# Performance work log

Measured on AMD Instinct MI355X. Metric: run time of the kernel, lower is better.

## Reference

```python
import jax, jax.numpy as jnp
import numpy as np

MIN_V, MAX_V = 1e-7, 10.0
POWER = 2.0
N_NODES = 200000


def _hyper_layer(H, edges, W, b):
    """One HyperTensorGraphConvolution layer (full-neighborhood branch).

    H: [N, d] node signals; edges: [E, S] node indices per hyperedge.
    For each (edge, node_i): power-mean over the other S-1 nodes of the edge,
    divided by (S-1), accumulated onto node_i; then row-normalize and linear.
    """
    N, d = H.shape
    E, S = edges.shape
    H = jnp.clip(H, MIN_V, MAX_V)
    P = H ** POWER                                   # [N, d]
    g = P[edges]                                     # [E, S, d] gather
    edge_sum = g.sum(axis=1, keepdims=True)          # [E, 1, d]
    neigh_mean = (edge_sum - g) / (S - 1)            # exclude self, /(len(nodes)-1)
    contrib = neigh_mean ** (1.0 / POWER)            # [E, S, d]
    add = jax.ops.segment_sum(contrib.reshape(E * S, d),
                              edges.reshape(-1), num_segments=N)
    new_signal = H + add
    # row-normalize (rowsum > 0 because H >= 1e-7)
    rowsum = new_signal.sum(axis=1)
    r_inv = jnp.where(jnp.isfinite(1.0 / rowsum), 1.0 / rowsum, 0.0)
    AH = new_signal * r_inv[:, None]
    return AH @ W + b


def setup_inputs() -> dict:
    key = jax.random.key(0)
    k1, k2, k3, k4, k5, k6 = jax.random.split(key, 6)
    d, h, c = 128, 16, 40
    H = jax.random.uniform(k1, (N_NODES, d), dtype=jnp.float32)
    edges = jax.random.randint(k2, (40000, 16), 0, N_NODES, dtype=jnp.int64)
    std1 = 1.0 / np.sqrt(h)
    std2 = 1.0 / np.sqrt(c)
    W1 = jax.random.uniform(k3, (d, h), jnp.float32, -std1, std1)
    b1 = jax.random.uniform(k4, (h,), jnp.float32, -std1, std1)
    W2 = jax.random.uniform(k5, (h, c), jnp.float32, -std2, std2)
    b2 = jax.random.uniform(k6, (c,), jnp.float32, -std2, std2)
    return {"H": H, "W1": W1, "b1": b1, "W2": W2, "b2": b2, "edges": edges}


def reference(H, W1, b1, W2, b2, edges):
    # layer 1 + relu (dropout is identity in eval mode)
    x = jax.nn.relu(_hyper_layer(H, edges, W1, b1))
    # layer 2
    return _hyper_layer(x, edges, W2, b2)
```

## Files before the change

### kernel.cpp

```cpp
#include <hip/hip_runtime.h>

#define MIN_V 1e-7f
#define MAX_V 10.0f
#define INV15 (1.0f/15.0f)
#define CAP 32

typedef _Float16 half2v __attribute__((ext_vector_type(2)));
typedef _Float16 half4v __attribute__((ext_vector_type(4)));
typedef _Float16 half8v __attribute__((ext_vector_type(8)));

static __device__ __forceinline__ float clipv(float v){
    return fminf(fmaxf(v, MIN_V), MAX_V);
}

__global__ __launch_bounds__(256) void ch_stream(const float* __restrict__ H,
                                                 _Float16* __restrict__ CH, int total8){
    int stride = gridDim.x*256;
    for (int i = blockIdx.x*256 + threadIdx.x; i < total8; i += stride){
        const float4* p = (const float4*)(H + (size_t)i*8);
        float4 a = p[0], b = p[1];
        half8v o;
        o[0]=(_Float16)clipv(a.x); o[1]=(_Float16)clipv(a.y);
        o[2]=(_Float16)clipv(a.z); o[3]=(_Float16)clipv(a.w);
        o[4]=(_Float16)clipv(b.x); o[5]=(_Float16)clipv(b.y);
        o[6]=(_Float16)clipv(b.z); o[7]=(_Float16)clipv(b.w);
        *(half8v*)(CH + (size_t)i*8) = o;
    }
}

__global__ void build_lists(const int* __restrict__ edges, int* __restrict__ cnt,
                            unsigned short* __restrict__ lists, int total){
    int i = blockIdx.x*256 + threadIdx.x;
    if (i >= total) return;
    int node = edges[i];
    int p = atomicAdd(&cnt[node], 1);
    if (p < CAP) lists[(size_t)node*CAP + p] = (unsigned short)(i >> 4);
}

__global__ __launch_bounds__(256) void es_l1(const _Float16* __restrict__ CH,
                                             const int* __restrict__ edges,
                                             _Float16* __restrict__ ES1s, int E){
    int tid = threadIdx.x;
    int hw = tid >> 5, l32 = tid & 31;
    int e = blockIdx.x*8 + hw;
    if (e >= E) return;
    int nid = edges[(size_t)e*16 + (l32 & 15)];
    int dq = l32 * 4;
    float s0=0.f, s1=0.f, s2=0.f, s3=0.f;
    #pragma unroll
    for (int s=0;s<16;++s){
        int idx = __shfl(nid, s, 32);
        half4v v = *(const half4v*)(CH + (size_t)idx*128 + dq);
        float f0=(float)v[0], f1=(float)v[1], f2=(float)v[2], f3=(float)v[3];
        s0 += f0*f0; s1 += f1*f1; s2 += f2*f2; s3 += f3*f3;
    }
    half4v o;
    o[0]=(_Float16)(s0*INV15); o[1]=(_Float16)(s1*INV15);
    o[2]=(_Float16)(s2*INV15); o[3]=(_Float16)(s3*INV15);
    *(half4v*)(ES1s + (size_t)e*128 + dq) = o;
}

__global__ __launch_bounds__(256) void fused_l1(
    const _Float16* __restrict__ CH, const _Float16* __restrict__ ES1s,
    const int* __restrict__ cnt, const unsigned short* __restrict__ lists,
    const float* __restrict__ W1, const float* __restrict__ b1,
    _Float16* __restrict__ X, int N, int EZERO){
    __shared__ _Float16 snw[2][8*128];
    int tid = threadIdx.x;
    int wave = tid >> 6, lane = tid & 63;

    int q = lane >> 4, h = lane & 15;
    half2v w2[16];
    #pragma unroll
    for (int i=0;i<16;++i){
        w2[i][0] = (_Float16)W1[(q*32+2*i  )*16 + h];
        w2[i][1] = (_Float16)W1[(q*32+2*i+1)*16 + h];
    }
    const half2v ones = {(_Float16)1.f, (_Float16)1.f};
    float bv = b1[h];

    int hw = tid >> 5;
    int k32 = tid & 31;
    int dq = k32 * 4;

    const _Float16 i15 = (_Float16)INV15;
    const half4v i15v = {i15, i15, i15, i15};
    const half4v z4 = {(_Float16)0.f,(_Float16)0.f,(_Float16)0.f,(_Float16)0.f};

    int nchunks = (N + 7) >> 3;
    int parity = 0;
    for (int chunk = blockIdx.x; chunk < nchunks; chunk += gridDim.x, parity ^= 1){
        int nb = chunk * 8;
        _Float16* sbuf = &snw[parity][0];

        int n = nb + hw;
        if (n < N){
            int len = cnt[n]; if (len > CAP) len = CAP;
            int myid = (int)lists[(size_t)n*CAP + k32];
            myid = (k32 < len) ? myid : EZERO;

            half4v hv = *(const half4v*)(CH + (size_t)n*128 + dq);
            half4v p16 = (hv * hv) * i15v;

            float a0=0.f, a1=0.f, a2=0.f, a3=0.f;
            for (int k0=0;k0<len;k0+=4){
                int e0 = __shfl(myid, k0,   32);
                int e1 = __shfl(myid, k0+1, 32);
                int e2 = __shfl(myid, k0+2, 32);
                int e3 = __shfl(myid, k0+3, 32);
                half4v v0 = *(const half4v*)(ES1s + (size_t)e0*128 + dq);
                half4v v1 = *(const half4v*)(ES1s + (size_t)e1*128 + dq);
                half4v v2 = *(const half4v*)(ES1s + (size_t)e2*128 + dq);
                half4v v3 = *(const half4v*)(ES1s + (size_t)e3*128 + dq);
                half4v s0 = __builtin_elementwise_sqrt(__builtin_elementwise_max(v0 - p16, z4));
                half4v s1 = __builtin_elementwise_sqrt(__builtin_elementwise_max(v1 - p16, z4));
                half4v s2 = __builtin_elementwise_sqrt(__builtin_elementwise_max(v2 - p16, z4));
                half4v s3 = __builtin_elementwise_sqrt(__builtin_elementwise_max(v3 - p16, z4));
                a0 += ((float)s0[0] + (float)s1[0]) + ((float)s2[0] + (float)s3[0]);
                a1 += ((float)s0[1] + (float)s1[1]) + ((float)s2[1] + (float)s3[1]);
                a2 += ((float)s0[2] + (float)s1[2]) + ((float)s2[2] + (float)s3[2]);
                a3 += ((float)s0[3] + (float)s1[3]) + ((float)s2[3] + (float)s3[3]);
            }
            half4v o;
            o[0] = (_Float16)((float)hv[0] + a0);
            o[1] = (_Float16)((float)hv[1] + a1);
            o[2] = (_Float16)((float)hv[2] + a2);
            o[3] = (_Float16)((float)hv[3] + a3);
            *(half4v*)&sbuf[hw*128 + dq] = o;
        }
        __syncthreads();

        #pragma unroll
        for (int r=0;r<2;++r){
            int nl = wave*2 + r;
            int n2 = nb + nl;
            if (n2 >= N) continue;
            float acc = 0.f, rs = 0.f;
            #pragma unroll
            for (int j=0;j<8;++j){
                half4v v = *(const half4v*)&sbuf[nl*128 + q*32 + j*4];
                half2v lo = {v[0], v[1]}, hi = {v[2], v[3]};
                acc = __builtin_amdgcn_fdot2(lo, w2[j*2  ], acc, false);
                acc = __builtin_amdgcn_fdot2(hi, w2[j*2+1], acc, false);
                rs  = __builtin_amdgcn_fdot2(lo, ones, rs, false);
                rs  = __builtin_amdgcn_fdot2(hi, ones, rs, false);
            }
            acc += __shfl_xor(acc, 16, 64);
            rs  += __shfl_xor(rs , 16, 64);
            acc += __shfl_xor(acc, 32, 64);
            rs  += __shfl_xor(rs , 32, 64);
            if (q == 0){
                float o = acc * __builtin_amdgcn_rcpf(rs) + bv;
                X[(size_t)n2*16 + h] = (_Float16)fmaxf(o, 0.f);
            }
        }
    }
}

__global__ __launch_bounds__(256) void es_l2(const _Float16* __restrict__ X,
                                             const int* __restrict__ edges,
                                             _Float16* __restrict__ ES2s, int E){
    int t = blockIdx.x*256 + threadIdx.x;
    int e = t >> 2, dq = (t & 3)*4;
    if (e >= E) return;
    const int* row = edges + (size_t)e*16;
    const _Float16 c7 = (_Float16)1e-7f;
    const half4v c7v = {c7, c7, c7, c7};
    float s0=0.f, s1=0.f, s2=0.f, s3=0.f;
    #pragma unroll
    for (int s=0;s<16;++s){
        half4v v = *(const half4v*)(X + (size_t)row[s]*16 + dq);
        v = __builtin_elementwise_max(v, c7v);
        float f0=(float)v[0], f1=(float)v[1], f2=(float)v[2], f3=(float)v[3];
        s0 += f0*f0; s1 += f1*f1; s2 += f2*f2; s3 += f3*f3;
    }
    half4v o;
    o[0]=(_Float16)(s0*INV15); o[1]=(_Float16)(s1*INV15);
    o[2]=(_Float16)(s2*INV15); o[3]=(_Float16)(s3*INV15);
    *(half4v*)(ES2s + (size_t)e*16 + dq) = o;
}

__global__ __launch_bounds__(256) void node_l2(
    const _Float16* __restrict__ X, const _Float16* __restrict__ ES2s,
    const int* __restrict__ cnt, const unsigned short* __restrict__ lists,
    const float* __restrict__ W2, const float* __restrict__ b2,
    float* __restrict__ out, int N, int EZERO){
    __shared__ half2v sW2h[8*40];
    __shared__ float sb[40];
    for (int i=threadIdx.x;i<320;i+=256){
        int d2 = i/40, c = i - d2*40;
        half2v wp;
        wp[0] = (_Float16)W2[(2*d2  )*40 + c];
        wp[1] = (_Float16)W2[(2*d2+1)*40 + c];
        sW2h[i] = wp;
    }
    if (threadIdx.x < 40) sb[threadIdx.x] = b2[threadIdx.x];
    __syncthreads();
    int n = blockIdx.x*256 + threadIdx.x;
    if (n >= N) return;

    const _Float16 c7 = (_Float16)1e-7f;
    const half8v c7v = {c7,c7,c7,c7,c7,c7,c7,c7};
    const half8v z8 = {(_Float16)0.f,(_Float16)0.f,(_Float16)0.f,(_Float16)0.f,
                       (_Float16)0.f,(_Float16)0.f,(_Float16)0.f,(_Float16)0.f};
    const _Float16 i15 = (_Float16)INV15;
    const half8v i15v = {i15,i15,i15,i15,i15,i15,i15,i15};

    const half8v* xr = (const half8v*)(X + (size_t)n*16);
    half8v x0 = __builtin_elementwise_max(xr[0], c7v);
    half8v x1 = __builtin_elementwise_max(xr[1], c7v);
    half8v ps0 = (x0*x0)*i15v;
    half8v ps1 = (x1*x1)*i15v;

    float xc[16], ad[16];
    #pragma unroll
    for (int d=0;d<8;++d){ xc[d]=(float)x0[d]; xc[8+d]=(float)x1[d]; ad[d]=0.f; ad[8+d]=0.f; }

    int len = cnt[n]; if (len > CAP) len = CAP;
    const unsigned short* lrow = lists + (size_t)n*CAP;
    for (int k0=0;k0<len;k0+=4){
        int e0 = (int)lrow[k0];
        int e1 = (k0+1 < len) ? (int)lrow[k0+1] : EZERO;
        int e2 = (k0+2 < len) ? (int)lrow[k0+2] : EZERO;
        int e3 = (k0+3 < len) ? (int)lrow[k0+3] : EZERO;
        const half8v* r0 = (const half8v*)(ES2s + (size_t)e0*16);
        const half8v* r1 = (const half8v*)(ES2s + (size_t)e1*16);
        const half8v* r2 = (const half8v*)(ES2s + (size_t)e2*16);
        const half8v* r3 = (const half8v*)(ES2s + (size_t)e3*16);
        half8v sa0 = __builtin_elementwise_sqrt(__builtin_elementwise_max(r0[0]-ps0, z8));
        half8v sb0 = __builtin_elementwise_sqrt(__builtin_elementwise_max(r0[1]-ps1, z8));
        half8v sa1 = __builtin_elementwise_sqrt(__builtin_elementwise_max(r1[0]-ps0, z8));
        half8v sb1 = __builtin_elementwise_sqrt(__builtin_elementwise_max(r1[1]-ps1, z8));
        half8v sa2 = __builtin_elementwise_sqrt(__builtin_elementwise_max(r2[0]-ps0, z8));
        half8v sb2 = __builtin_elementwise_sqrt(__builtin_elementwise_max(r2[1]-ps1, z8));
        half8v sa3 = __builtin_elementwise_sqrt(__builtin_elementwise_max(r3[0]-ps0, z8));
        half8v sb3 = __builtin_elementwise_sqrt(__builtin_elementwise_max(r3[1]-ps1, z8));
        #pragma unroll
        for (int d=0;d<8;++d){
            ad[d]   += ((float)sa0[d] + (float)sa1[d]) + ((float)sa2[d] + (float)sa3[d]);
            ad[8+d] += ((float)sb0[d] + (float)sb1[d]) + ((float)sb2[d] + (float)sb3[d]);
        }
    }
    float rs = 0.f;
    float nw[16];
    #pragma unroll
    for (int d=0;d<16;++d){ nw[d] = xc[d] + ad[d]; rs += nw[d]; }
    float rinv = __builtin_amdgcn_rcpf(rs);

    half2v nwh[8];
    #pragma unroll
    for (int i=0;i<8;++i){ nwh[i][0] = (_Float16)nw[2*i]; nwh[i][1] = (_Float16)nw[2*i+1]; }

    float4 ob[10];
    #pragma unroll
    for (int c=0;c<40;++c){
        float acc = 0.f;
        #pragma unroll
        for (int d2=0;d2<8;++d2)
            acc = __builtin_amdgcn_fdot2(nwh[d2], sW2h[d2*40+c], acc, false);
        ((float*)ob)[c] = rinv*acc + sb[c];
    }
    float4* op = (float4*)(out + (size_t)n*40);
    #pragma unroll
    for (int j=0;j<10;++j) op[j] = ob[j];
}

extern "C" void kernel_launch(void* const* d_in, const int* in_sizes, int n_in,
                              void* d_out, int out_size, void* d_ws, size_t ws_size,
                              hipStream_t stream){
    (void)n_in; (void)out_size; (void)ws_size;
    const float* H  = (const float*)d_in[0];
    const float* W1 = (const float*)d_in[1];
    const float* b1 = (const float*)d_in[2];
    const float* W2 = (const float*)d_in[3];
    const float* b2 = (const float*)d_in[4];
    const int* edges = (const int*)d_in[5];
    float* out = (float*)d_out;

    const int N = in_sizes[0] / 128;
    const int E = in_sizes[5] / 16;
    const int total = E * 16;
    const int total8 = N * 128 / 8;

    char* ws = (char*)d_ws;
    size_t off = 0;
    _Float16* CH   = (_Float16*)(ws + off);
    _Float16* ES2s = (_Float16*)(ws + off);
    off += (size_t)N*128*sizeof(_Float16);
    _Float16* ES1s = (_Float16*)(ws + off); off += (size_t)(E+1)*128*sizeof(_Float16);
    _Float16* X    = (_Float16*)(ws + off); off += (size_t)N*16*sizeof(_Float16);
    int* cnt = (int*)(ws + off); off += (size_t)N*sizeof(int);
    unsigned short* lists = (unsigned short*)(ws + off);
    off += (size_t)N*CAP*sizeof(unsigned short);

    hipMemsetAsync(cnt, 0, (size_t)N*sizeof(int), stream);
    hipMemsetAsync(ES1s + (size_t)E*128, 0, 128*sizeof(_Float16), stream);
    ch_stream<<<2048, 256, 0, stream>>>(H, CH, total8);
    build_lists<<<(total+255)/256, 256, 0, stream>>>(edges, cnt, lists, total);
    es_l1<<<(E+7)/8, 256, 0, stream>>>(CH, edges, ES1s, E);
    fused_l1<<<2048, 256, 0, stream>>>(CH, ES1s, cnt, lists, W1, b1, X, N, E);
    hipMemsetAsync(ES2s + (size_t)E*16, 0, 16*sizeof(_Float16), stream);
    es_l2<<<(E*4+255)/256, 256, 0, stream>>>(X, edges, ES2s, E);
    node_l2<<<(N+255)/256, 256, 0, stream>>>(X, ES2s, cnt, lists, W2, b2, out, N, E);
}
```

Before: 203.6 us.

## Widen es_l1 loads, unroll fused_l1 gather by 8, split node_l2 across thread pairs

es_l1 now assigns 16 lanes per hyperedge, each loading 8 halfs at once, instead of 32 lanes with 4-half loads. The fused_l1 neighbor loop issues 8 gathers before any compute, to keep more memory requests in flight. node_l2 splits each node's work across two adjacent threads, one per 8-feature half. The partial row sums and the half-precision features are exchanged with xor-shuffles, and each thread computes and stores 20 of the 40 outputs. The aim is more memory-level parallelism and occupancy on gather-bound kernels, at the cost of extra shuffles and duplicated list reads in node_l2.

```diff
diff --git a/kernel.cpp b/kernel.cpp
--- a/kernel.cpp
+++ b/kernel.cpp
@@ -11,6 +11,11 @@
 
 static __device__ __forceinline__ float clipv(float v){
     return fminf(fmaxf(v, MIN_V), MAX_V);
+}
+static __device__ __forceinline__ half2v shflx1(half2v v){
+    int i = __builtin_bit_cast(int, v);
+    i = __shfl_xor(i, 1, 64);
+    return __builtin_bit_cast(half2v, i);
 }
 
 __global__ __launch_bounds__(256) void ch_stream(const float* __restrict__ H,
@@ -41,23 +46,24 @@
                                              const int* __restrict__ edges,
                                              _Float16* __restrict__ ES1s, int E){
     int tid = threadIdx.x;
-    int hw = tid >> 5, l32 = tid & 31;
-    int e = blockIdx.x*8 + hw;
+    int sub = tid & 15;
+    int e = blockIdx.x*16 + (tid >> 4);
     if (e >= E) return;
-    int nid = edges[(size_t)e*16 + (l32 & 15)];
-    int dq = l32 * 4;
-    float s0=0.f, s1=0.f, s2=0.f, s3=0.f;
-    #pragma unroll
-    for (int s=0;s<16;++s){
-        int idx = __shfl(nid, s, 32);
-        half4v v = *(const half4v*)(CH + (size_t)idx*128 + dq);
-        float f0=(float)v[0], f1=(float)v[1], f2=(float)v[2], f3=(float)v[3];
-        s0 += f0*f0; s1 += f1*f1; s2 += f2*f2; s3 += f3*f3;
-    }
-    half4v o;
-    o[0]=(_Float16)(s0*INV15); o[1]=(_Float16)(s1*INV15);
-    o[2]=(_Float16)(s2*INV15); o[3]=(_Float16)(s3*INV15);
-    *(half4v*)(ES1s + (size_t)e*128 + dq) = o;
+    int nid = edges[(size_t)e*16 + sub];
+    float s[8];
+    #pragma unroll
+    for (int j=0;j<8;++j) s[j] = 0.f;
+    #pragma unroll
+    for (int t=0;t<16;++t){
+        int idx = __shfl(nid, t, 16);
+        half8v v = *(const half8v*)(CH + (size_t)idx*128 + sub*8);
+        #pragma unroll
+        for (int j=0;j<8;++j){ float f = (float)v[j]; s[j] += f*f; }
+    }
+    half8v o;
+    #pragma unroll
+    for (int j=0;j<8;++j) o[j] = (_Float16)(s[j]*INV15);
+    *(half8v*)(ES1s + (size_t)e*128 + sub*8) = o;
 }
 
 __global__ __launch_bounds__(256) void fused_l1(
@@ -103,23 +109,21 @@
             half4v p16 = (hv * hv) * i15v;
 
             float a0=0.f, a1=0.f, a2=0.f, a3=0.f;
-            for (int k0=0;k0<len;k0+=4){
-                int e0 = __shfl(myid, k0,   32);
-                int e1 = __shfl(myid, k0+1, 32);
-                int e2 = __shfl(myid, k0+2, 32);
-                int e3 = __shfl(myid, k0+3, 32);
-                half4v v0 = *(const half4v*)(ES1s + (size_t)e0*128 + dq);
-                half4v v1 = *(const half4v*)(ES1s + (size_t)e1*128 + dq);
-                half4v v2 = *(const half4v*)(ES1s + (size_t)e2*128 + dq);
-                half4v v3 = *(const half4v*)(ES1s + (size_t)e3*128 + dq);
-                half4v s0 = __builtin_elementwise_sqrt(__builtin_elementwise_max(v0 - p16, z4));
-                half4v s1 = __builtin_elementwise_sqrt(__builtin_elementwise_max(v1 - p16, z4));
-                half4v s2 = __builtin_elementwise_sqrt(__builtin_elementwise_max(v2 - p16, z4));
-                half4v s3 = __builtin_elementwise_sqrt(__builtin_elementwise_max(v3 - p16, z4));
-                a0 += ((float)s0[0] + (float)s1[0]) + ((float)s2[0] + (float)s3[0]);
-                a1 += ((float)s0[1] + (float)s1[1]) + ((float)s2[1] + (float)s3[1]);
-                a2 += ((float)s0[2] + (float)s1[2]) + ((float)s2[2] + (float)s3[2]);
-                a3 += ((float)s0[3] + (float)s1[3]) + ((float)s2[3] + (float)s3[3]);
+            for (int k0=0;k0<len;k0+=8){
+                half4v v[8];
+                #pragma unroll
+                for (int j=0;j<8;++j){
+                    int e = __shfl(myid, k0+j, 32);
+                    v[j] = *(const half4v*)(ES1s + (size_t)e*128 + dq);
+                }
+                #pragma unroll
+                for (int j=0;j<8;++j){
+                    half4v sq = __builtin_elementwise_sqrt(__builtin_elementwise_max(v[j] - p16, z4));
+                    a0 += (float)sq[0];
+                    a1 += (float)sq[1];
+                    a2 += (float)sq[2];
+                    a3 += (float)sq[3];
+                }
             }
             half4v o;
             o[0] = (_Float16)((float)hv[0] + a0);
@@ -196,7 +200,8 @@
     }
     if (threadIdx.x < 40) sb[threadIdx.x] = b2[threadIdx.x];
     __syncthreads();
-    int n = blockIdx.x*256 + threadIdx.x;
+    int t = blockIdx.x*256 + threadIdx.x;
+    int n = t >> 1, p = t & 1;
     if (n >= N) return;
 
     const _Float16 c7 = (_Float16)1e-7f;
@@ -206,15 +211,13 @@
     const _Float16 i15 = (_Float16)INV15;
     const half8v i15v = {i15,i15,i15,i15,i15,i15,i15,i15};
 
-    const half8v* xr = (const half8v*)(X + (size_t)n*16);
-    half8v x0 = __builtin_elementwise_max(xr[0], c7v);
-    half8v x1 = __builtin_elementwise_max(xr[1], c7v);
-    half8v ps0 = (x0*x0)*i15v;
-    half8v ps1 = (x1*x1)*i15v;
-
-    float xc[16], ad[16];
-    #pragma unroll
-    for (int d=0;d<8;++d){ xc[d]=(float)x0[d]; xc[8+d]=(float)x1[d]; ad[d]=0.f; ad[8+d]=0.f; }
+    half8v xh = *(const half8v*)(X + (size_t)n*16 + p*8);
+    xh = __builtin_elementwise_max(xh, c7v);
+    half8v ps = (xh*xh)*i15v;
+
+    float xc[8], ad[8];
+    #pragma unroll
+    for (int d=0;d<8;++d){ xc[d]=(float)xh[d]; ad[d]=0.f; }
 
     int len = cnt[n]; if (len > CAP) len = CAP;
     const unsigned short* lrow = lists + (size_t)n*CAP;
@@ -223,46 +226,52 @@
         int e1 = (k0+1 < len) ? (int)lrow[k0+1] : EZERO;
         int e2 = (k0+2 < len) ? (int)lrow[k0+2] : EZERO;
         int e3 = (k0+3 < len) ? (int)lrow[k0+3] : EZERO;
-        const half8v* r0 = (const half8v*)(ES2s + (size_t)e0*16);
-        const half8v* r1 = (const half8v*)(ES2s + (size_t)e1*16);
-        const half8v* r2 = (const half8v*)(ES2s + (size_t)e2*16);
-        const half8v* r3 = (const half8v*)(ES2s + (size_t)e3*16);
-        half8v sa0 = __builtin_elementwise_sqrt(__builtin_elementwise_max(r0[0]-ps0, z8));
-        half8v sb0 = __builtin_elementwise_sqrt(__builtin_elementwise_max(r0[1]-ps1, z8));
-        half8v sa1 = __builtin_elementwise_sqrt(__builtin_elementwise_max(r1[0]-ps0, z8));
-        half8v sb1 = __builtin_elementwise_sqrt(__builtin_elementwise_max(r1[1]-ps1, z8));
-        half8v sa2 = __builtin_elementwise_sqrt(__builtin_elementwise_max(r2[0]-ps0, z8));
-        half8v sb2 = __builtin_elementwise_sqrt(__builtin_elementwise_max(r2[1]-ps1, z8));
-        half8v sa3 = __builtin_elementwise_sqrt(__builtin_elementwise_max(r3[0]-ps0, z8));
-        half8v sb3 = __builtin_elementwise_sqrt(__builtin_elementwise_max(r3[1]-ps1, z8));
+        half8v r0 = *(const half8v*)(ES2s + (size_t)e0*16 + p*8);
+        half8v r1 = *(const half8v*)(ES2s + (size_t)e1*16 + p*8);
+        half8v r2 = *(const half8v*)(ES2s + (size_t)e2*16 + p*8);
+        half8v r3 = *(const half8v*)(ES2s + (size_t)e3*16 + p*8);
+        half8v s0 = __builtin_elementwise_sqrt(__builtin_elementwise_max(r0-ps, z8));
+        half8v s1 = __builtin_elementwise_sqrt(__builtin_elementwise_max(r1-ps, z8));
+        half8v s2 = __builtin_elementwise_sqrt(__builtin_elementwise_max(r2-ps, z8));
+        half8v s3 = __builtin_elementwise_sqrt(__builtin_elementwise_max(r3-ps, z8));
         #pragma unroll
-        for (int d=0;d<8;++d){
-            ad[d]   += ((float)sa0[d] + (float)sa1[d]) + ((float)sa2[d] + (float)sa3[d]);
-            ad[8+d] += ((float)sb0[d] + (float)sb1[d]) + ((float)sb2[d] + (float)sb3[d]);
-        }
-    }
-    float rs = 0.f;
-    float nw[16];
-    #pragma unroll
-    for (int d=0;d<16;++d){ nw[d] = xc[d] + ad[d]; rs += nw[d]; }
+        for (int d=0;d<8;++d)
+            ad[d] += ((float)s0[d] + (float)s1[d]) + ((float)s2[d] + (float)s3[d]);
+    }
+    float rsl = 0.f;
+    float nw[8];
+    #pragma unroll
+    for (int d=0;d<8;++d){ nw[d] = xc[d] + ad[d]; rsl += nw[d]; }
+    float rs = rsl + __shfl_xor(rsl, 1, 64);
     float rinv = __builtin_amdgcn_rcpf(rs);
 
-    half2v nwh[8];
-    #pragma unroll
-    for (int i=0;i<8;++i){ nwh[i][0] = (_Float16)nw[2*i]; nwh[i][1] = (_Float16)nw[2*i+1]; }
-
-    float4 ob[10];
-    #pragma unroll
-    for (int c=0;c<40;++c){
+    half2v mine[4], oth[4];
+    #pragma unroll
+    for (int i=0;i<4;++i){
+        mine[i][0] = (_Float16)nw[2*i];
+        mine[i][1] = (_Float16)nw[2*i+1];
+        oth[i] = shflx1(mine[i]);
+    }
+    half2v all8[8];
+    #pragma unroll
+    for (int i=0;i<4;++i){
+        all8[4*p + i]     = mine[i];
+        all8[4*(1-p) + i] = oth[i];
+    }
+
+    float ob[20];
+    #pragma unroll
+    for (int c=0;c<20;++c){
+        int col = p*20 + c;
         float acc = 0.f;
         #pragma unroll
         for (int d2=0;d2<8;++d2)
-            acc = __builtin_amdgcn_fdot2(nwh[d2], sW2h[d2*40+c], acc, false);
-        ((float*)ob)[c] = rinv*acc + sb[c];
-    }
-    float4* op = (float4*)(out + (size_t)n*40);
-    #pragma unroll
-    for (int j=0;j<10;++j) op[j] = ob[j];
+            acc = __builtin_amdgcn_fdot2(all8[d2], sW2h[d2*40+col], acc, false);
+        ob[c] = rinv*acc + sb[col];
+    }
+    float4* op = (float4*)(out + (size_t)n*40 + p*20);
+    #pragma unroll
+    for (int j=0;j<5;++j) op[j] = ((float4*)ob)[j];
 }
 
 extern "C" void kernel_launch(void* const* d_in, const int* in_sizes, int n_in,
@@ -297,9 +306,9 @@
     hipMemsetAsync(ES1s + (size_t)E*128, 0, 128*sizeof(_Float16), stream);
     ch_stream<<<2048, 256, 0, stream>>>(H, CH, total8);
     build_lists<<<(total+255)/256, 256, 0, stream>>>(edges, cnt, lists, total);
-    es_l1<<<(E+7)/8, 256, 0, stream>>>(CH, edges, ES1s, E);
+    es_l1<<<(E+15)/16, 256, 0, stream>>>(CH, edges, ES1s, E);
     fused_l1<<<2048, 256, 0, stream>>>(CH, ES1s, cnt, lists, W1, b1, X, N, E);
     hipMemsetAsync(ES2s + (size_t)E*16, 0, 16*sizeof(_Float16), stream);
     es_l2<<<(E*4+255)/256, 256, 0, stream>>>(X, edges, ES2s, E);
-    node_l2<<<(N+255)/256, 256, 0, stream>>>(X, ES2s, cnt, lists, W2, b2, out, N, E);
-}
+    node_l2<<<(N*2+255)/256, 256, 0, stream>>>(X, ES2s, cnt, lists, W2, b2, out, N, E);
+}
```

Result: slower. 210.0 us (+3.1%).
